# Kernel optimization log

Hardware: AMD Instinct MI355X
Metric: run time of the kernel (lower is better)

The kernel has to match this reference:

```python
import jax, jax.numpy as jnp
import numpy as np


def setup_inputs() -> dict:
    key = jax.random.key(0)
    k1, k2, k3, k4 = jax.random.split(key, 4)
    N, C, H, W = 1, 512, 192, 192
    F, K = 512, 3
    x = jax.random.normal(k1, (N, C, H, W), dtype=jnp.float32)
    w = jax.random.normal(k2, (F, C, K, K), dtype=jnp.float32) * 0.05
    b = jax.random.normal(k3, (F,), dtype=jnp.float32)
    # binary RoI mask over output spatial grid (stands in for PIL polygon raster)
    mask = jax.random.randint(k4, (H, W), 0, 2, dtype=jnp.int32)
    return {"x": x, "w": w, "b": b, "mask": mask}


def reference(x, w, b, mask):
    # my_conv: im2col conv (stride=1, pad=1), gather rows where mask==1,
    # GEMM, scatter back into zeros, then add bias everywhere (res += b
    # happens AFTER the scatter). Equivalent dense form: conv(x,w)*mask + b.
    conv = jax.lax.conv_general_dilated(
        x, w,
        window_strides=(1, 1),
        padding=((1, 1), (1, 1)),
        dimension_numbers=("NCHW", "OIHW", "NCHW"),
    )  # [N, F, H, W]
    m = mask.astype(conv.dtype)[None, None, :, :]
    return conv * m + b[None, :, None, None]
```

## Files before the change

### kernel.cpp

```cpp
#include <hip/hip_runtime.h>


typedef unsigned short ushort_t;
typedef __attribute__((ext_vector_type(8))) __bf16 bf16x8;
typedef __attribute__((ext_vector_type(4))) float f32x4;
typedef __attribute__((ext_vector_type(8))) unsigned short ushort8;

#define IMG_W 192
#define IMG_H 192
#define HW    36864
#define PAD_W 194
#define C_IN  512
#define F_OUT 512
#define KTOT  4608

__device__ __forceinline__ unsigned short f2bf(float f) {
  unsigned int u = __builtin_bit_cast(unsigned int, f);
  u += 0x7fffu + ((u >> 16) & 1u);
  return (unsigned short)(u >> 16);
}

__device__ __forceinline__ void async16(const void* g, void* l) {
  __builtin_amdgcn_global_load_lds(
      (const __attribute__((address_space(1))) unsigned int*)g,
      (__attribute__((address_space(3))) unsigned int*)l, 16, 0, 0);
}

__global__ void halo_zero(ushort_t* __restrict__ Xt) {
  int p = blockIdx.x;
  int r, c;
  if (p < 388) { r = (p >= 194) ? 193 : 0; c = (p >= 194) ? p - 194 : p; }
  else         { int q = p - 388; r = 1 + (q >> 1); c = (q & 1) ? 193 : 0; }
  unsigned int* dst = (unsigned int*)(Xt + ((size_t)r * PAD_W + c) * C_IN);
  dst[threadIdx.x] = 0;
}

__global__ void prep_x(const float* __restrict__ x, ushort_t* __restrict__ Xt) {
  __shared__ float tile[64][65];
  const int tid = threadIdx.x;
  const int h  = blockIdx.z;
  const int w0 = blockIdx.x * 64;
  const int c0 = blockIdx.y * 64;

  const int wl_r = tid & 63;
  const int cg_r = tid >> 6;
  const float* src = x + (size_t)(c0 + cg_r * 16) * HW + (size_t)h * IMG_W + w0 + wl_r;
#pragma unroll
  for (int cc = 0; cc < 16; ++cc)
    tile[cg_r * 16 + cc][wl_r] = src[(size_t)cc * HW];
  __syncthreads();

  const int wl = tid >> 2;
  const int cg = tid & 3;
  ushort_t* dst = Xt + ((size_t)(h + 1) * PAD_W + (w0 + wl + 1)) * C_IN + c0 + cg * 16;
  ushort8 v0, v1;
#pragma unroll
  for (int cc = 0; cc < 8; ++cc) v0[cc] = f2bf(tile[cg * 16 + cc][wl]);
#pragma unroll
  for (int cc = 0; cc < 8; ++cc) v1[cc] = f2bf(tile[cg * 16 + 8 + cc][wl]);
  *(ushort8*)dst = v0;
  *(ushort8*)(dst + 8) = v1;
}

__global__ void prep_w(const float* __restrict__ w, ushort_t* __restrict__ Wt) {
  const int idx = blockIdx.x * 256 + threadIdx.x;
  const int f = idx >> 9;
  const int c = idx & 511;
  const float* src = w + (size_t)idx * 9;
  float v[9];
#pragma unroll
  for (int t = 0; t < 9; ++t) v[t] = src[t];
  ushort_t* dst = Wt + (size_t)f * KTOT + c;
#pragma unroll
  for (int t = 0; t < 9; ++t) dst[t * C_IN] = f2bf(v[t]);
}

__global__ void compact(const int* __restrict__ mask, int* __restrict__ list,
                        int* __restrict__ counter) {
  const int i = blockIdx.x * 256 + threadIdx.x;
  const int lane = threadIdx.x & 63;
  const int m = mask[i];
  unsigned long long b = __ballot(m != 0);
  int base = 0;
  if (lane == 0 && b) base = atomicAdd(counter, __popcll(b));
  base = __shfl(base, 0);
  if (m) list[base + __popcll(b & ((1ull << lane) - 1ull))] = i;
}

__global__ void bias_fill(const int* __restrict__ mask, const float* __restrict__ bias,
                          float* __restrict__ out) {
  const int n = (blockIdx.x * 256 + threadIdx.x) * 4;
  const int f = blockIdx.y;
  const float bv = bias[f];
  const int4 m = *(const int4*)(mask + n);
  float* o = out + (size_t)f * HW + n;
  if (!m.x) o[0] = bv;
  if (!m.y) o[1] = bv;
  if (!m.z) o[2] = bv;
  if (!m.w) o[3] = bv;
}

__global__ __launch_bounds__(256) void conv_gemm(
    const ushort_t* __restrict__ Wt, const ushort_t* __restrict__ Xt,
    const float* __restrict__ bias, const int* __restrict__ list,
    const int* __restrict__ counter, float* __restrict__ out) {
  __shared__ __align__(16) ushort_t As[128 * 32];
  __shared__ __align__(16) ushort_t Bs[128 * 32];

  const int count = counter[0];
  const int n0 = blockIdx.x * 128;
  if (n0 >= count) return;

  const int tid  = threadIdx.x;
  const int lane = tid & 63;
  const int wave = tid >> 6;
  const int wm   = wave >> 1;
  const int wn   = wave & 1;
  const int m0   = blockIdx.y * 128;

  const int nl = tid >> 2;
  const int kq_log = (tid & 3) ^ ((tid >> 3) & 3);
  const int posA = n0 + nl;
  const int posB = posA + 64;
  const int pixA = (posA < count) ? list[posA] : 0;
  const int pixB = (posB < count) ? list[posB] : 0;
  const int ha = pixA / IMG_W, wa = pixA - ha * IMG_W;
  const int hb = pixB / IMG_W, wb = pixB - hb * IMG_W;
  const ushort_t* bSrcA = Xt + ((size_t)(ha + 1) * PAD_W + (wa + 1)) * C_IN + kq_log * 8;
  const ushort_t* bSrcB = Xt + ((size_t)(hb + 1) * PAD_W + (wb + 1)) * C_IN + kq_log * 8;
  const ushort_t* aSrcA = Wt + (size_t)(m0 + nl) * KTOT + kq_log * 8;
  const ushort_t* aSrcB = aSrcA + (size_t)64 * KTOT;

  ushort_t* aDstA = &As[wave * 512];
  ushort_t* aDstB = &As[2048 + wave * 512];
  ushort_t* bDstA = &Bs[wave * 512];
  ushort_t* bDstB = &Bs[2048 + wave * 512];

  f32x4 acc[4][4] = {};

  const int col   = lane & 15;
  const int quad  = lane >> 4;
  const int physq = quad ^ ((col >> 1) & 3);
  const int aOff  = (wm * 64 + col) * 32 + physq * 8;
  const int bOff  = (wn * 64 + col) * 32 + physq * 8;

#pragma unroll 1
  for (int tap = 0; tap < 9; ++tap) {
    const int toff = ((tap / 3) * PAD_W + (tap % 3) - (PAD_W + 1)) * C_IN;
    const ushort_t* bA = bSrcA + toff;
    const ushort_t* bB = bSrcB + toff;
    const ushort_t* aA = aSrcA + tap * 512;
    const ushort_t* aB = aSrcB + tap * 512;
#pragma unroll 1
    for (int kc = 0; kc < 512; kc += 32) {
      async16(aA + kc, aDstA);
      async16(aB + kc, aDstB);
      async16(bA + kc, bDstA);
      async16(bB + kc, bDstB);
      __syncthreads();

      bf16x8 af[4], bfr[4];
#pragma unroll
      for (int i = 0; i < 4; ++i) af[i]  = *(const bf16x8*)&As[aOff + i * 512];
#pragma unroll
      for (int j = 0; j < 4; ++j) bfr[j] = *(const bf16x8*)&Bs[bOff + j * 512];
#pragma unroll
      for (int i = 0; i < 4; ++i)
#pragma unroll
        for (int j = 0; j < 4; ++j)
          acc[i][j] = __builtin_amdgcn_mfma_f32_16x16x32_bf16(af[i], bfr[j], acc[i][j], 0, 0, 0);
      __syncthreads();
    }
  }

#pragma unroll
  for (int j = 0; j < 4; ++j) {
    const int pos = n0 + wn * 64 + j * 16 + col;
    if (pos < count) {
      const int n_pix = list[pos];
#pragma unroll
      for (int i = 0; i < 4; ++i) {
        const int mrow = m0 + wm * 64 + i * 16 + quad * 4;
        float* o = out + (size_t)mrow * HW + n_pix;
#pragma unroll
        for (int r = 0; r < 4; ++r)
          o[(size_t)r * HW] = acc[i][j][r] + bias[mrow + r];
      }
    }
  }
}

extern "C" void kernel_launch(void* const* d_in, const int* in_sizes, int n_in,
                              void* d_out, int out_size, void* d_ws, size_t ws_size,
                              hipStream_t stream) {
  const float* x    = (const float*)d_in[0];
  const float* w    = (const float*)d_in[1];
  const float* bias = (const float*)d_in[2];
  const int*   mask = (const int*)d_in[3];
  float* out = (float*)d_out;

  int* list    = (int*)d_ws;
  int* counter = list + HW;
  ushort_t* Xt = (ushort_t*)((char*)d_ws + 147712);
  ushort_t* Wt = Xt + (size_t)PAD_W * PAD_W * C_IN;

  hipMemsetAsync(counter, 0, sizeof(int), stream);
  compact<<<dim3(HW / 256), 256, 0, stream>>>(mask, list, counter);
  halo_zero<<<dim3(772), 256, 0, stream>>>(Xt);
  prep_x<<<dim3(3, 8, 192), 256, 0, stream>>>(x, Xt);
  prep_w<<<dim3((F_OUT * C_IN) / 256), 256, 0, stream>>>(w, Wt);
  bias_fill<<<dim3(HW / 1024, F_OUT), 256, 0, stream>>>(mask, bias, out);
  conv_gemm<<<dim3((HW + 127) / 128, F_OUT / 128), 256, 0, stream>>>(
      Wt, Xt, bias, list, counter, out);
}
```

Baseline: 307.0 us.

## Fuse prep kernels into one launch and deepen GEMM K-step with prefetch

Merges halo zeroing, x/w conversion, counter reset and a full unconditional bias fill into one prep kernel, removing several launches and the memset. The conv GEMM now uses a 64-wide K step with an XOR-swizzled LDS layout and issues the next tile's async loads right after reading fragments, so loads overlap the MFMAs. Launch bounds request 3 blocks per SM. Bias is written everywhere before the GEMM overwrites masked pixels, which doubles some output writes but removes the mask read.

```diff
diff --git a/kernel.cpp b/kernel.cpp
--- a/kernel.cpp
+++ b/kernel.cpp
@@ -26,53 +26,65 @@
       (__attribute__((address_space(3))) unsigned int*)l, 16, 0, 0);
 }
 
-__global__ void halo_zero(ushort_t* __restrict__ Xt) {
-  int p = blockIdx.x;
-  int r, c;
-  if (p < 388) { r = (p >= 194) ? 193 : 0; c = (p >= 194) ? p - 194 : p; }
-  else         { int q = p - 388; r = 1 + (q >> 1); c = (q & 1) ? 193 : 0; }
-  unsigned int* dst = (unsigned int*)(Xt + ((size_t)r * PAD_W + c) * C_IN);
-  dst[threadIdx.x] = 0;
-}
-
-__global__ void prep_x(const float* __restrict__ x, ushort_t* __restrict__ Xt) {
+__global__ void prep_all(const float* __restrict__ x, const float* __restrict__ w,
+                         const float* __restrict__ bias,
+                         ushort_t* __restrict__ Xt, ushort_t* __restrict__ Wt,
+                         int* __restrict__ counter, float* __restrict__ out) {
   __shared__ float tile[64][65];
+  const int bid = blockIdx.x;
   const int tid = threadIdx.x;
-  const int h  = blockIdx.z;
-  const int w0 = blockIdx.x * 64;
-  const int c0 = blockIdx.y * 64;
-
-  const int wl_r = tid & 63;
-  const int cg_r = tid >> 6;
-  const float* src = x + (size_t)(c0 + cg_r * 16) * HW + (size_t)h * IMG_W + w0 + wl_r;
-#pragma unroll
-  for (int cc = 0; cc < 16; ++cc)
-    tile[cg_r * 16 + cc][wl_r] = src[(size_t)cc * HW];
-  __syncthreads();
-
-  const int wl = tid >> 2;
-  const int cg = tid & 3;
-  ushort_t* dst = Xt + ((size_t)(h + 1) * PAD_W + (w0 + wl + 1)) * C_IN + c0 + cg * 16;
-  ushort8 v0, v1;
-#pragma unroll
-  for (int cc = 0; cc < 8; ++cc) v0[cc] = f2bf(tile[cg * 16 + cc][wl]);
-#pragma unroll
-  for (int cc = 0; cc < 8; ++cc) v1[cc] = f2bf(tile[cg * 16 + 8 + cc][wl]);
-  *(ushort8*)dst = v0;
-  *(ushort8*)(dst + 8) = v1;
-}
-
-__global__ void prep_w(const float* __restrict__ w, ushort_t* __restrict__ Wt) {
-  const int idx = blockIdx.x * 256 + threadIdx.x;
-  const int f = idx >> 9;
-  const int c = idx & 511;
-  const float* src = w + (size_t)idx * 9;
-  float v[9];
-#pragma unroll
-  for (int t = 0; t < 9; ++t) v[t] = src[t];
-  ushort_t* dst = Wt + (size_t)f * KTOT + c;
-#pragma unroll
-  for (int t = 0; t < 9; ++t) dst[t * C_IN] = f2bf(v[t]);
+
+  if (bid < 4608) {
+    const int p  = bid;
+    const int w0 = (p % 3) * 64;
+    const int c0 = ((p / 3) & 7) * 64;
+    const int h  = p / 24;
+
+    const int wl_r = tid & 63;
+    const int cg_r = tid >> 6;
+    const float* src = x + (size_t)(c0 + cg_r * 16) * HW + (size_t)h * IMG_W + w0 + wl_r;
+#pragma unroll
+    for (int cc = 0; cc < 16; ++cc)
+      tile[cg_r * 16 + cc][wl_r] = src[(size_t)cc * HW];
+    __syncthreads();
+
+    const int wl = tid >> 2;
+    const int cg = tid & 3;
+    ushort_t* dst = Xt + ((size_t)(h + 1) * PAD_W + (w0 + wl + 1)) * C_IN + c0 + cg * 16;
+    ushort8 v0, v1;
+#pragma unroll
+    for (int cc = 0; cc < 8; ++cc) v0[cc] = f2bf(tile[cg * 16 + cc][wl]);
+#pragma unroll
+    for (int cc = 0; cc < 8; ++cc) v1[cc] = f2bf(tile[cg * 16 + 8 + cc][wl]);
+    *(ushort8*)dst = v0;
+    *(ushort8*)(dst + 8) = v1;
+  } else if (bid < 5380) {
+    const int p = bid - 4608;
+    int r, c;
+    if (p < 388) { r = (p >= 194) ? 193 : 0; c = (p >= 194) ? p - 194 : p; }
+    else         { int q = p - 388; r = 1 + (q >> 1); c = (q & 1) ? 193 : 0; }
+    unsigned int* dst = (unsigned int*)(Xt + ((size_t)r * PAD_W + c) * C_IN);
+    dst[tid] = 0;
+  } else if (bid < 6404) {
+    const int idx = (bid - 5380) * 256 + tid;
+    const int f = idx >> 9;
+    const int c = idx & 511;
+    const float* src = w + (size_t)idx * 9;
+    float v[9];
+#pragma unroll
+    for (int t = 0; t < 9; ++t) v[t] = src[t];
+    ushort_t* dst = Wt + (size_t)f * KTOT + c;
+#pragma unroll
+    for (int t = 0; t < 9; ++t) dst[t * C_IN] = f2bf(v[t]);
+  } else if (bid == 6404) {
+    if (tid == 0) *counter = 0;
+  } else {
+    const int n4 = (bid - 6405) * 256 + tid;
+    const int f  = n4 / (HW / 4);
+    const int r4 = n4 - f * (HW / 4);
+    f32x4 bv = {bias[f], bias[f], bias[f], bias[f]};
+    *(f32x4*)(out + (size_t)f * HW + (size_t)r4 * 4) = bv;
+  }
 }
 
 __global__ void compact(const int* __restrict__ mask, int* __restrict__ list,
@@ -87,25 +99,12 @@
   if (m) list[base + __popcll(b & ((1ull << lane) - 1ull))] = i;
 }
 
-__global__ void bias_fill(const int* __restrict__ mask, const float* __restrict__ bias,
-                          float* __restrict__ out) {
-  const int n = (blockIdx.x * 256 + threadIdx.x) * 4;
-  const int f = blockIdx.y;
-  const float bv = bias[f];
-  const int4 m = *(const int4*)(mask + n);
-  float* o = out + (size_t)f * HW + n;
-  if (!m.x) o[0] = bv;
-  if (!m.y) o[1] = bv;
-  if (!m.z) o[2] = bv;
-  if (!m.w) o[3] = bv;
-}
-
-__global__ __launch_bounds__(256) void conv_gemm(
+__global__ __launch_bounds__(256, 3) void conv_gemm(
     const ushort_t* __restrict__ Wt, const ushort_t* __restrict__ Xt,
     const float* __restrict__ bias, const int* __restrict__ list,
     const int* __restrict__ counter, float* __restrict__ out) {
-  __shared__ __align__(16) ushort_t As[128 * 32];
-  __shared__ __align__(16) ushort_t Bs[128 * 32];
+  __shared__ __align__(16) ushort_t As[128 * 64];
+  __shared__ __align__(16) ushort_t Bs[128 * 64];
 
   const int count = counter[0];
   const int n0 = blockIdx.x * 128;
@@ -118,59 +117,75 @@
   const int wn   = wave & 1;
   const int m0   = blockIdx.y * 128;
 
-  const int nl = tid >> 2;
-  const int kq_log = (tid & 3) ^ ((tid >> 3) & 3);
-  const int posA = n0 + nl;
-  const int posB = posA + 64;
-  const int pixA = (posA < count) ? list[posA] : 0;
-  const int pixB = (posB < count) ? list[posB] : 0;
-  const int ha = pixA / IMG_W, wa = pixA - ha * IMG_W;
-  const int hb = pixB / IMG_W, wb = pixB - hb * IMG_W;
-  const ushort_t* bSrcA = Xt + ((size_t)(ha + 1) * PAD_W + (wa + 1)) * C_IN + kq_log * 8;
-  const ushort_t* bSrcB = Xt + ((size_t)(hb + 1) * PAD_W + (wb + 1)) * C_IN + kq_log * 8;
-  const ushort_t* aSrcA = Wt + (size_t)(m0 + nl) * KTOT + kq_log * 8;
-  const ushort_t* aSrcB = aSrcA + (size_t)64 * KTOT;
-
-  ushort_t* aDstA = &As[wave * 512];
-  ushort_t* aDstB = &As[2048 + wave * 512];
-  ushort_t* bDstA = &Bs[wave * 512];
-  ushort_t* bDstB = &Bs[2048 + wave * 512];
+  const int rrel = lane >> 3;
+  const int q    = (lane & 7) ^ rrel;
+
+  const ushort_t* aSrc = Wt + (size_t)(m0 + wave * 32 + rrel) * KTOT + q * 8;
+
+  unsigned int bOffs[4];
+#pragma unroll
+  for (int ii = 0; ii < 4; ++ii) {
+    const int pos = n0 + wave * 32 + ii * 8 + rrel;
+    const int pix = (pos < count) ? list[pos] : 0;
+    const int hh = pix / IMG_W, ww = pix - hh * IMG_W;
+    bOffs[ii] = ((hh + 1) * PAD_W + (ww + 1)) * C_IN + q * 8;
+  }
+
+  ushort_t* aDst = &As[wave * 32 * 64];
+  ushort_t* bDst = &Bs[wave * 32 * 64];
+
+  const int col  = lane & 15;
+  const int quad = lane >> 4;
 
   f32x4 acc[4][4] = {};
 
-  const int col   = lane & 15;
-  const int quad  = lane >> 4;
-  const int physq = quad ^ ((col >> 1) & 3);
-  const int aOff  = (wm * 64 + col) * 32 + physq * 8;
-  const int bOff  = (wn * 64 + col) * 32 + physq * 8;
+  {
+    const int toff0 = -(PAD_W + 1) * C_IN;
+#pragma unroll
+    for (int ii = 0; ii < 4; ++ii) {
+      async16(aSrc + (size_t)ii * 8 * KTOT, aDst + ii * 512);
+      async16(Xt + (int)bOffs[ii] + toff0, bDst + ii * 512);
+    }
+  }
 
 #pragma unroll 1
-  for (int tap = 0; tap < 9; ++tap) {
-    const int toff = ((tap / 3) * PAD_W + (tap % 3) - (PAD_W + 1)) * C_IN;
-    const ushort_t* bA = bSrcA + toff;
-    const ushort_t* bB = bSrcB + toff;
-    const ushort_t* aA = aSrcA + tap * 512;
-    const ushort_t* aB = aSrcB + tap * 512;
-#pragma unroll 1
-    for (int kc = 0; kc < 512; kc += 32) {
-      async16(aA + kc, aDstA);
-      async16(aB + kc, aDstB);
-      async16(bA + kc, bDstA);
-      async16(bB + kc, bDstB);
+  for (int kk = 0; kk < 72; ++kk) {
+    __syncthreads();
+    bf16x8 af[2][4], bfr[2][4];
+#pragma unroll
+    for (int s = 0; s < 2; ++s) {
+#pragma unroll
+      for (int i = 0; i < 4; ++i) {
+        const int row = wm * 64 + i * 16 + col;
+        af[s][i] = *(const bf16x8*)&As[row * 64 + ((s * 4 + quad) ^ (row & 7)) * 8];
+      }
+#pragma unroll
+      for (int j = 0; j < 4; ++j) {
+        const int row = wn * 64 + j * 16 + col;
+        bfr[s][j] = *(const bf16x8*)&Bs[row * 64 + ((s * 4 + quad) ^ (row & 7)) * 8];
+      }
+    }
+    if (kk < 71) {
       __syncthreads();
-
-      bf16x8 af[4], bfr[4];
-#pragma unroll
-      for (int i = 0; i < 4; ++i) af[i]  = *(const bf16x8*)&As[aOff + i * 512];
-#pragma unroll
-      for (int j = 0; j < 4; ++j) bfr[j] = *(const bf16x8*)&Bs[bOff + j * 512];
+      const int kn   = kk + 1;
+      const int tapn = kn >> 3;
+      const int kcn  = (kn & 7) * 64;
+      const int toffn = ((tapn / 3) * PAD_W + (tapn % 3) - (PAD_W + 1)) * C_IN;
+      const int aoffn = tapn * 512 + kcn;
+#pragma unroll
+      for (int ii = 0; ii < 4; ++ii) {
+        async16(aSrc + (size_t)ii * 8 * KTOT + aoffn, aDst + ii * 512);
+        async16(Xt + (int)bOffs[ii] + toffn + kcn, bDst + ii * 512);
+      }
+    }
+#pragma unroll
+    for (int s = 0; s < 2; ++s)
 #pragma unroll
       for (int i = 0; i < 4; ++i)
 #pragma unroll
         for (int j = 0; j < 4; ++j)
-          acc[i][j] = __builtin_amdgcn_mfma_f32_16x16x32_bf16(af[i], bfr[j], acc[i][j], 0, 0, 0);
-      __syncthreads();
-    }
+          acc[i][j] = __builtin_amdgcn_mfma_f32_16x16x32_bf16(af[s][i], bfr[s][j],
+                                                              acc[i][j], 0, 0, 0);
   }
 
 #pragma unroll
@@ -204,12 +219,8 @@
   ushort_t* Xt = (ushort_t*)((char*)d_ws + 147712);
   ushort_t* Wt = Xt + (size_t)PAD_W * PAD_W * C_IN;
 
-  hipMemsetAsync(counter, 0, sizeof(int), stream);
+  prep_all<<<dim3(24837), 256, 0, stream>>>(x, w, bias, Xt, Wt, counter, out);
   compact<<<dim3(HW / 256), 256, 0, stream>>>(mask, list, counter);
-  halo_zero<<<dim3(772), 256, 0, stream>>>(Xt);
-  prep_x<<<dim3(3, 8, 192), 256, 0, stream>>>(x, Xt);
-  prep_w<<<dim3((F_OUT * C_IN) / 256), 256, 0, stream>>>(w, Wt);
-  bias_fill<<<dim3(HW / 1024, F_OUT), 256, 0, stream>>>(mask, bias, out);
   conv_gemm<<<dim3((HW + 127) / 128, F_OUT / 128), 256, 0, stream>>>(
       Wt, Xt, bias, list, counter, out);
 }
```

Result: faster. 264.5 us (-13.8%).
